# Performance work log

Measured on AMD Instinct MI355X. Metric: run time of the kernel, lower is better.

The kernel has to match this reference:

```python
import jax, jax.numpy as jnp
import numpy as np

N_NODES = 10000
N_EDGES = 80000
IN_DIM, HID, OUT_DIM, HEADS = 768, 512, 768, 4
NEG_SLOPE = 0.2


def setup_inputs() -> dict:
    key = jax.random.key(0)
    ks = jax.random.split(key, 10)
    g = 0.05
    return {
        "x": jax.random.normal(ks[0], (N_NODES, IN_DIM), jnp.float32),
        "edge_index": jax.random.randint(ks[1], (2, N_EDGES), 0, N_NODES, jnp.int64),
        # layer 1: GATConv(768 -> 512, heads=4, concat=True)
        "W1": jax.random.normal(ks[2], (IN_DIM, HEADS * HID), jnp.float32) * g,
        "a1_src": jax.random.normal(ks[3], (HEADS, HID), jnp.float32) * g,
        "a1_dst": jax.random.normal(ks[4], (HEADS, HID), jnp.float32) * g,
        "b1": jnp.zeros((HEADS * HID,), jnp.float32),
        # layer 2: GATConv(2048 -> 768, heads=1, concat=False)
        "W2": jax.random.normal(ks[5], (HEADS * HID, OUT_DIM), jnp.float32) * g,
        "a2_src": jax.random.normal(ks[6], (1, OUT_DIM), jnp.float32) * g,
        "a2_dst": jax.random.normal(ks[7], (1, OUT_DIM), jnp.float32) * g,
        "b2": jnp.zeros((OUT_DIM,), jnp.float32),
    }


def _gat_layer(x, src, dst, W, a_src, a_dst, b, heads, d_out, concat):
    N = x.shape[0]
    h = (x @ W).reshape(N, heads, d_out)              # [N, H, D]
    as_n = jnp.einsum('nhd,hd->nh', h, a_src)          # [N, H]
    ad_n = jnp.einsum('nhd,hd->nh', h, a_dst)
    e = jax.nn.leaky_relu(as_n[src] + ad_n[dst], NEG_SLOPE)  # [E, H]
    # segment softmax over destination nodes
    e_max = jax.lax.stop_gradient(jax.ops.segment_max(e, dst, num_segments=N))
    ex = jnp.exp(e - e_max[dst])
    denom = jax.ops.segment_sum(ex, dst, num_segments=N)
    alpha = ex / (denom[dst] + 1e-16)                  # [E, H]
    msg = alpha[:, :, None] * h[src]                   # [E, H, D]
    out = jax.ops.segment_sum(msg, dst, num_segments=N)  # [N, H, D]
    out = out.reshape(N, heads * d_out) if concat else out.mean(axis=1)
    return out + b


def reference(x, edge_index, W1, a1_src, a1_dst, b1, W2, a2_src, a2_dst, b2):
    N = x.shape[0]
    # PyG GATConv default: add self-loops
    loops = jnp.arange(N, dtype=edge_index.dtype)
    src = jnp.concatenate([edge_index[0], loops])
    dst = jnp.concatenate([edge_index[1], loops])
    h = _gat_layer(x, src, dst, W1, a1_src, a1_dst, b1, HEADS, HID, True)
    h = jax.nn.elu(h)
    out = _gat_layer(h, src, dst, W2, a2_src, a2_dst, b2, 1, OUT_DIM, False)
    return out
```

## Files before the change

kernel.cpp:

```cpp
#include <hip/hip_runtime.h>
#include <hip/hip_bf16.h>

#define N_NODES 10000
#define E_REAL  80000
#define E_TOTAL 90000
#define IN_DIM  768
#define HID     512
#define HEADS   4
#define OUT_DIM 768
#define HD1     (HEADS * HID)
#define NEG_SLOPE 0.2f
#define H1_HSTRIDE (N_NODES * HID)

typedef unsigned short ushort_t;
typedef unsigned int uint_t;

__device__ inline float b2f(ushort_t u) { return __uint_as_float(((uint_t)u) << 16); }
__device__ inline ushort_t f2b(float f) {
    __hip_bfloat16 h = __float2bfloat16(f);
    return *reinterpret_cast<ushort_t*>(&h);
}

__device__ inline void edge_sd(const int* __restrict__ ei, int e, int& s, int& d) {
    if (e < E_REAL) { s = ei[e]; d = ei[E_REAL + e]; }
    else            { s = e - E_REAL; d = s; }
}

#define GLDS(g, l) __builtin_amdgcn_global_load_lds( \
    (const __attribute__((address_space(1))) void*)(g), \
    (__attribute__((address_space(3))) void*)(l), 16, 0, 0)

static const long B_H1B  = 0L;
static const long B_HB   = 40960000L;
static const long B_XB   = 81920000L;
static const long B_W1T  = 97280000L;
static const long B_W2T  = 100425728L;
static const long B_SM   = 103571456L;
static const long SM_AS1   = 0;
static const long SM_AD1   = 40000;
static const long SM_DEN1  = 120000;
static const long SM_E1    = 160000;
static const long SM_AS2   = 520000;
static const long SM_AD2   = 530000;
static const long SM_DEN2  = 550000;
static const long SM_E2    = 560000;
static const long SM_CNT   = 650000;
static const long SM_ROWS  = 660000;
static const long SM_CURS  = 670016;
static const long SM_END   = 680032;
static const long B_CSRS = B_SM + SM_END * 4;
static const long B_CSRE = B_CSRS + 360000L;

__global__ __launch_bounds__(256)
void cast_bf16(const float* __restrict__ in, ushort_t* __restrict__ o, long n) {
    long i = ((long)blockIdx.x * 256 + threadIdx.x) * 8;
    if (i >= n) return;
    float4 v0 = *(const float4*)(in + i);
    float4 v1 = *(const float4*)(in + i + 4);
    ushort_t r[8] = {f2b(v0.x), f2b(v0.y), f2b(v0.z), f2b(v0.w),
                     f2b(v1.x), f2b(v1.y), f2b(v1.z), f2b(v1.w)};
    *(uint4*)(o + i) = *(uint4*)r;
}

__global__ __launch_bounds__(256)
void cast_transpose(const float* __restrict__ W, ushort_t* __restrict__ WT,
                    int K, int N) {
    __shared__ ushort_t t[32][33];
    const int n0 = blockIdx.x * 32, k0 = blockIdx.y * 32;
    const int tx = threadIdx.x & 31, ty = threadIdx.x >> 5;
#pragma unroll
    for (int i = 0; i < 4; ++i) {
        int k = ty + i * 8;
        t[k][tx] = f2b(W[(long)(k0 + k) * N + n0 + tx]);
    }
    __syncthreads();
#pragma unroll
    for (int i = 0; i < 4; ++i) {
        int n = ty + i * 8;
        WT[(long)(n0 + n) * K + k0 + tx] = t[tx][n];
    }
}

typedef short bf16x8 __attribute__((ext_vector_type(8)));
typedef float f32x4 __attribute__((ext_vector_type(4)));

#define BM 128
#define BN 128
#define BK 32

template<int CMODE>
__global__ __launch_bounds__(256)
void gemm_bf16(const ushort_t* __restrict__ A, const ushort_t* __restrict__ BT,
               ushort_t* __restrict__ C, int M, int N, int K) {
    __shared__ ushort_t As[BM * BK];
    __shared__ ushort_t Bs[BN * BK];
    const int tid  = threadIdx.x;
    const int wave = tid >> 6, lane = tid & 63;
    const int quad = lane >> 4, l16 = lane & 15;
    const int bm = blockIdx.y * BM, bn = blockIdx.x * BN;
    const int wr = (wave >> 1) * 64, wc = (wave & 1) * 64;

    const int ch0 = wave * 128 + lane;
    const int ch1 = ch0 + 64;
    const int r0 = ch0 >> 2, c0 = (ch0 & 3) ^ ((r0 >> 1) & 3);
    const int r1 = ch1 >> 2, c1 = (ch1 & 3) ^ ((r1 >> 1) & 3);
    const ushort_t* a0 = A + (long)(bm + r0) * K + c0 * 8;
    const ushort_t* a1 = A + (long)(bm + r1) * K + c1 * 8;
    const ushort_t* b0 = BT + (long)(bn + r0) * K + c0 * 8;
    const ushort_t* b1 = BT + (long)(bn + r1) * K + c1 * 8;
    ushort_t* lA0 = As + (wave * 128) * 8;
    ushort_t* lA1 = As + (wave * 128 + 64) * 8;
    ushort_t* lB0 = Bs + (wave * 128) * 8;
    ushort_t* lB1 = Bs + (wave * 128 + 64) * 8;

    const int swz = (l16 >> 1) & 3;
    f32x4 acc[4][4] = {};

    for (int k0 = 0; k0 < K; k0 += BK) {
        GLDS(a0 + k0, lA0);
        GLDS(a1 + k0, lA1);
        GLDS(b0 + k0, lB0);
        GLDS(b1 + k0, lB1);
        __syncthreads();
        bf16x8 af[4], bfr[4];
#pragma unroll
        for (int i = 0; i < 4; ++i) {
            af[i]  = *(const bf16x8*)(As + ((wr + i * 16 + l16) * 4 + (quad ^ swz)) * 8);
            bfr[i] = *(const bf16x8*)(Bs + ((wc + i * 16 + l16) * 4 + (quad ^ swz)) * 8);
        }
#pragma unroll
        for (int i = 0; i < 4; ++i)
#pragma unroll
            for (int j = 0; j < 4; ++j)
                acc[i][j] = __builtin_amdgcn_mfma_f32_16x16x32_bf16(
                    af[i], bfr[j], acc[i][j], 0, 0, 0);
        __syncthreads();
    }

#pragma unroll
    for (int i = 0; i < 4; ++i) {
#pragma unroll
        for (int r = 0; r < 4; ++r) {
            int row = bm + wr + i * 16 + quad * 4 + r;
            if (row >= M) continue;
#pragma unroll
            for (int j = 0; j < 4; ++j) {
                int col = bn + wc + j * 16 + l16;
                if (CMODE == 0) {
                    C[(long)row * N + col] = f2b(acc[i][j][r]);
                } else {
                    C[(long)(col >> 9) * H1_HSTRIDE + (long)row * HID + (col & 511)]
                        = f2b(acc[i][j][r]);
                }
            }
        }
    }
}

__global__ __launch_bounds__(256)
void attn1(const ushort_t* __restrict__ h, const float* __restrict__ a_s,
           const float* __restrict__ a_d, float* __restrict__ os,
           float* __restrict__ od) {
    const int n = blockIdx.x;
    const int w = threadIdx.x >> 6, lane = threadIdx.x & 63;
    uint4 hv = *(const uint4*)(h + (long)w * H1_HSTRIDE + (long)n * HID + lane * 8);
    const float* asp = a_s + w * HID + lane * 8;
    const float* adp = a_d + w * HID + lane * 8;
    const ushort_t* pb = (const ushort_t*)&hv;
    float ps = 0.f, pd = 0.f;
#pragma unroll
    for (int c = 0; c < 8; ++c) {
        float v = b2f(pb[c]);
        ps += v * asp[c];
        pd += v * adp[c];
    }
#pragma unroll
    for (int off = 32; off > 0; off >>= 1) {
        ps += __shfl_down(ps, off);
        pd += __shfl_down(pd, off);
    }
    if (lane == 0) { os[n * HEADS + w] = ps; od[n * HEADS + w] = pd; }
}

__global__ __launch_bounds__(256)
void attn2(const ushort_t* __restrict__ h, const float* __restrict__ a_s,
           const float* __restrict__ a_d, float* __restrict__ os,
           float* __restrict__ od) {
    __shared__ float rs[4], rd[4];
    const int n = blockIdx.x, tid = threadIdx.x;
    const int w = tid >> 6, lane = tid & 63;
    float ps = 0.f, pd = 0.f;
#pragma unroll
    for (int j = 0; j < 3; ++j) {
        int c = tid + j * 256;
        float v = b2f(h[(long)n * OUT_DIM + c]);
        ps += v * a_s[c];
        pd += v * a_d[c];
    }
#pragma unroll
    for (int off = 32; off > 0; off >>= 1) {
        ps += __shfl_down(ps, off);
        pd += __shfl_down(pd, off);
    }
    if (lane == 0) { rs[w] = ps; rd[w] = pd; }
    __syncthreads();
    if (tid == 0) {
        os[n] = rs[0] + rs[1] + rs[2] + rs[3];
        od[n] = rd[0] + rd[1] + rd[2] + rd[3];
    }
}

__global__ __launch_bounds__(256)
void edge_soft(const int* __restrict__ ei, int H,
               const float* __restrict__ as_n, const float* __restrict__ ad_n,
               float* __restrict__ ebuf, float* __restrict__ denom) {
    int idx = blockIdx.x * 256 + threadIdx.x;
    if (idx >= E_TOTAL * H) return;
    int e = idx / H, hh = idx - e * H;
    int s, d; edge_sd(ei, e, s, d);
    float v = as_n[(long)s * H + hh] + ad_n[(long)d * H + hh];
    v = v > 0.f ? v : NEG_SLOPE * v;
    float ex = expf(v);
    ebuf[idx] = ex;
    atomicAdd(&denom[(long)d * H + hh], ex);
}

__global__ __launch_bounds__(256)
void hist_dst(const int* __restrict__ ei, int* __restrict__ cnt) {
    int e = blockIdx.x * 256 + threadIdx.x;
    if (e >= E_TOTAL) return;
    int s, d; edge_sd(ei, e, s, d);
    atomicAdd(&cnt[d], 1);
}

#define SCAN_CH 40
__global__ __launch_bounds__(256)
void scan_nodes(const int* __restrict__ cnt, int* __restrict__ rows,
                int* __restrict__ curs) {
    __shared__ int part[256];
    const int tid = threadIdx.x;
    const int base = tid * SCAN_CH;
    int local[SCAN_CH];
    int sum = 0;
#pragma unroll
    for (int i = 0; i < SCAN_CH; ++i) {
        int idx = base + i;
        int v = (idx < N_NODES) ? cnt[idx] : 0;
        local[i] = v; sum += v;
    }
    part[tid] = sum;
    __syncthreads();
    for (int off = 1; off < 256; off <<= 1) {
        int v = (tid >= off) ? part[tid - off] : 0;
        __syncthreads();
        part[tid] += v;
        __syncthreads();
    }
    int run = part[tid] - sum;
#pragma unroll
    for (int i = 0; i < SCAN_CH; ++i) {
        int idx = base + i;
        if (idx < N_NODES) { rows[idx] = run; curs[idx] = run; run += local[i]; }
    }
    if (tid == 255) rows[N_NODES] = run;
}

__global__ __launch_bounds__(256)
void scatter_edges(const int* __restrict__ ei, int* __restrict__ curs,
                   int* __restrict__ csr_src, int* __restrict__ csr_eid) {
    int e = blockIdx.x * 256 + threadIdx.x;
    if (e >= E_TOTAL) return;
    int s, d; edge_sd(ei, e, s, d);
    int pos = atomicAdd(&curs[d], 1);
    csr_src[pos] = s;
    csr_eid[pos] = e;
}

__global__ __launch_bounds__(64)
void agg1(const int* __restrict__ rows, const int* __restrict__ csr_src,
          const int* __restrict__ csr_eid, const float* __restrict__ ebuf,
          const float* __restrict__ denom, const ushort_t* __restrict__ hf,
          const float* __restrict__ b1, ushort_t* __restrict__ o) {
    const int n = blockIdx.x, hh = blockIdx.y, lane = threadIdx.x;
    const int beg = rows[n], end = rows[n + 1];
    const ushort_t* hsl = hf + (long)hh * H1_HSTRIDE;
    const float dinv = 1.f / (denom[(long)n * HEADS + hh] + 1e-16f);
    float acc[8] = {};
    for (int k = beg; k < end; k += 4) {
        int nk = end - k; if (nk > 4) nk = 4;
        uint4 v[4]; float al[4];
#pragma unroll
        for (int u = 0; u < 4; ++u) {
            if (u < nk) {
                int s = csr_src[k + u];
                al[u] = ebuf[(long)csr_eid[k + u] * HEADS + hh] * dinv;
                v[u]  = *(const uint4*)(hsl + (long)s * HID + lane * 8);
            }
        }
#pragma unroll
        for (int u = 0; u < 4; ++u) {
            if (u < nk) {
                const ushort_t* p = (const ushort_t*)&v[u];
#pragma unroll
                for (int c = 0; c < 8; ++c) acc[c] += al[u] * b2f(p[c]);
            }
        }
    }
    const float* bp = b1 + hh * HID + lane * 8;
    ushort_t r[8];
#pragma unroll
    for (int c = 0; c < 8; ++c) {
        float vv = acc[c] + bp[c];
        r[c] = f2b(vv > 0.f ? vv : expm1f(vv));
    }
    *(uint4*)(o + (long)n * HD1 + hh * HID + lane * 8) = *(uint4*)r;
}

__global__ __launch_bounds__(64)
void agg2(const int* __restrict__ rows, const int* __restrict__ csr_src,
          const int* __restrict__ csr_eid, const float* __restrict__ ebuf,
          const float* __restrict__ denom, const ushort_t* __restrict__ hf,
          const float* __restrict__ b2, float* __restrict__ out) {
    const int n = blockIdx.x, lane = threadIdx.x;
    const int beg = rows[n], end = rows[n + 1];
    const float dinv = 1.f / (denom[n] + 1e-16f);
    float acc[12] = {};
    for (int k = beg; k < end; k += 4) {
        int nk = end - k; if (nk > 4) nk = 4;
        uint4 v4[4]; uint2 v2[4]; float al[4];
#pragma unroll
        for (int u = 0; u < 4; ++u) {
            if (u < nk) {
                int s = csr_src[k + u];
                al[u] = ebuf[csr_eid[k + u]] * dinv;
                const ushort_t* hp = hf + (long)s * OUT_DIM;
                v4[u] = *(const uint4*)(hp + lane * 8);
                v2[u] = *(const uint2*)(hp + 512 + lane * 4);
            }
        }
#pragma unroll
        for (int u = 0; u < 4; ++u) {
            if (u < nk) {
                const ushort_t* p4 = (const ushort_t*)&v4[u];
                const ushort_t* p2 = (const ushort_t*)&v2[u];
#pragma unroll
                for (int c = 0; c < 8; ++c) acc[c] += al[u] * b2f(p4[c]);
#pragma unroll
                for (int c = 0; c < 4; ++c) acc[8 + c] += al[u] * b2f(p2[c]);
            }
        }
    }
    float* op = out + (long)n * OUT_DIM;
#pragma unroll
    for (int c = 0; c < 8; ++c) op[lane * 8 + c] = acc[c] + b2[lane * 8 + c];
#pragma unroll
    for (int c = 0; c < 4; ++c)
        op[512 + lane * 4 + c] = acc[8 + c] + b2[512 + lane * 4 + c];
}

extern "C" void kernel_launch(void* const* d_in, const int* in_sizes, int n_in,
                              void* d_out, int out_size, void* d_ws, size_t ws_size,
                              hipStream_t stream) {
    const float* x   = (const float*)d_in[0];
    const int*   ei  = (const int*)d_in[1];
    const float* W1  = (const float*)d_in[2];
    const float* a1s = (const float*)d_in[3];
    const float* a1d = (const float*)d_in[4];
    const float* b1  = (const float*)d_in[5];
    const float* W2  = (const float*)d_in[6];
    const float* a2s = (const float*)d_in[7];
    const float* a2d = (const float*)d_in[8];
    const float* b2  = (const float*)d_in[9];
    float* out = (float*)d_out;
    char* base = (char*)d_ws;

    ushort_t* h1b = (ushort_t*)(base + B_H1B);
    ushort_t* hb  = (ushort_t*)(base + B_HB);
    ushort_t* xb  = (ushort_t*)(base + B_XB);
    ushort_t* h2b = xb;
    ushort_t* w1t = (ushort_t*)(base + B_W1T);
    ushort_t* w2t = (ushort_t*)(base + B_W2T);
    float*    sm  = (float*)(base + B_SM);

    float* as1  = sm + SM_AS1;
    float* ad1  = sm + SM_AD1;
    float* den1 = sm + SM_DEN1;
    float* e1   = sm + SM_E1;
    float* as2  = sm + SM_AS2;
    float* ad2  = sm + SM_AD2;
    float* den2 = sm + SM_DEN2;
    float* e2   = sm + SM_E2;
    int* cnt    = (int*)(sm + SM_CNT);
    int* rows   = (int*)(sm + SM_ROWS);
    int* curs   = (int*)(sm + SM_CURS);
    int* csr_src = (int*)(base + B_CSRS);
    int* csr_eid = (int*)(base + B_CSRE);

    hipMemsetAsync(sm, 0, (size_t)(SM_CNT + 10000) * sizeof(float), stream);

    {
        long nx = (long)N_NODES * IN_DIM;
        cast_bf16<<<(int)(nx / 8 / 256 + 1), 256, 0, stream>>>(x, xb, nx);
        cast_transpose<<<dim3(HD1 / 32, IN_DIM / 32), 256, 0, stream>>>(W1, w1t, IN_DIM, HD1);
        cast_transpose<<<dim3(OUT_DIM / 32, HD1 / 32), 256, 0, stream>>>(W2, w2t, HD1, OUT_DIM);
        hist_dst<<<(E_TOTAL + 255) / 256, 256, 0, stream>>>(ei, cnt);
        scan_nodes<<<1, 256, 0, stream>>>(cnt, rows, curs);
        scatter_edges<<<(E_TOTAL + 255) / 256, 256, 0, stream>>>(ei, curs, csr_src, csr_eid);
    }

    gemm_bf16<1><<<dim3(HD1 / BN, (N_NODES + BM - 1) / BM), 256, 0, stream>>>(
        xb, w1t, h1b, N_NODES, HD1, IN_DIM);
    attn1<<<N_NODES, 256, 0, stream>>>(h1b, a1s, a1d, as1, ad1);
    {
        int total = E_TOTAL * HEADS;
        edge_soft<<<(total + 255) / 256, 256, 0, stream>>>(ei, HEADS, as1, ad1, e1, den1);
    }
    agg1<<<dim3(N_NODES, HEADS), 64, 0, stream>>>(rows, csr_src, csr_eid, e1, den1, h1b, b1, hb);

    gemm_bf16<0><<<dim3(OUT_DIM / BN, (N_NODES + BM - 1) / BM), 256, 0, stream>>>(
        hb, w2t, h2b, N_NODES, OUT_DIM, HD1);
    attn2<<<N_NODES, 256, 0, stream>>>(h2b, a2s, a2d, as2, ad2);
    {
        int total = E_TOTAL;
        edge_soft<<<(total + 255) / 256, 256, 0, stream>>>(ei, 1, as2, ad2, e2, den2);
    }
    agg2<<<N_NODES, 64, 0, stream>>>(rows, csr_src, csr_eid, e2, den2, h2b, b2, out);
}
```

Measured before the change: 364.8 us.

## Split GAT aggregation across edge groups and feature slices with shuffle reduction

Both aggregation kernels now place four nodes in each 256-thread block, one wave per node. Each wave splits into four 16-lane groups that take interleaved edges, and the blocks are also split across feature slices (4 slices for layer 1, 8 for layer 2). Partial sums are combined with cross-lane shuffles before one group writes the result. The aim is more memory-level parallelism per node and better occupancy for the gather-heavy loops, at the cost of more blocks re-reading CSR indices and attention weights, and of idle lanes in layer 2 (only 12 of 16 lanes active).

```diff
diff --git a/kernel.cpp b/kernel.cpp
--- a/kernel.cpp
+++ b/kernel.cpp
@@ -276,86 +276,80 @@
     csr_eid[pos] = e;
 }
 
-__global__ __launch_bounds__(64)
+__global__ __launch_bounds__(256)
 void agg1(const int* __restrict__ rows, const int* __restrict__ csr_src,
           const int* __restrict__ csr_eid, const float* __restrict__ ebuf,
           const float* __restrict__ denom, const ushort_t* __restrict__ hf,
           const float* __restrict__ b1, ushort_t* __restrict__ o) {
-    const int n = blockIdx.x, hh = blockIdx.y, lane = threadIdx.x;
+    const int sh = blockIdx.x & 3, nq = blockIdx.x >> 2;
+    const int hh = blockIdx.y;
+    const int wave = threadIdx.x >> 6, lane = threadIdx.x & 63;
+    const int grp = lane >> 4, l = lane & 15;
+    const int n = nq * 4 + wave;
     const int beg = rows[n], end = rows[n + 1];
-    const ushort_t* hsl = hf + (long)hh * H1_HSTRIDE;
+    const ushort_t* hsl = hf + (long)hh * H1_HSTRIDE + sh * 128;
     const float dinv = 1.f / (denom[(long)n * HEADS + hh] + 1e-16f);
     float acc[8] = {};
-    for (int k = beg; k < end; k += 4) {
-        int nk = end - k; if (nk > 4) nk = 4;
-        uint4 v[4]; float al[4];
-#pragma unroll
-        for (int u = 0; u < 4; ++u) {
-            if (u < nk) {
-                int s = csr_src[k + u];
-                al[u] = ebuf[(long)csr_eid[k + u] * HEADS + hh] * dinv;
-                v[u]  = *(const uint4*)(hsl + (long)s * HID + lane * 8);
-            }
+    for (int k = beg + grp; k < end; k += 4) {
+        int s = csr_src[k];
+        float al = ebuf[(long)csr_eid[k] * HEADS + hh] * dinv;
+        uint4 v = *(const uint4*)(hsl + (long)s * HID + l * 8);
+        const ushort_t* p = (const ushort_t*)&v;
+#pragma unroll
+        for (int c = 0; c < 8; ++c) acc[c] += al * b2f(p[c]);
+    }
+#pragma unroll
+    for (int c = 0; c < 8; ++c) {
+        acc[c] += __shfl_down(acc[c], 32);
+        acc[c] += __shfl_down(acc[c], 16);
+    }
+    if (grp == 0) {
+        const int ch = hh * HID + sh * 128 + l * 8;
+        const float* bp = b1 + ch;
+        ushort_t r[8];
+#pragma unroll
+        for (int c = 0; c < 8; ++c) {
+            float vv = acc[c] + bp[c];
+            r[c] = f2b(vv > 0.f ? vv : expm1f(vv));
         }
-#pragma unroll
-        for (int u = 0; u < 4; ++u) {
-            if (u < nk) {
-                const ushort_t* p = (const ushort_t*)&v[u];
-#pragma unroll
-                for (int c = 0; c < 8; ++c) acc[c] += al[u] * b2f(p[c]);
-            }
-        }
-    }
-    const float* bp = b1 + hh * HID + lane * 8;
-    ushort_t r[8];
-#pragma unroll
-    for (int c = 0; c < 8; ++c) {
-        float vv = acc[c] + bp[c];
-        r[c] = f2b(vv > 0.f ? vv : expm1f(vv));
-    }
-    *(uint4*)(o + (long)n * HD1 + hh * HID + lane * 8) = *(uint4*)r;
-}
-
-__global__ __launch_bounds__(64)
+        *(uint4*)(o + (long)n * HD1 + ch) = *(uint4*)r;
+    }
+}
+
+__global__ __launch_bounds__(256)
 void agg2(const int* __restrict__ rows, const int* __restrict__ csr_src,
           const int* __restrict__ csr_eid, const float* __restrict__ ebuf,
           const float* __restrict__ denom, const ushort_t* __restrict__ hf,
           const float* __restrict__ b2, float* __restrict__ out) {
-    const int n = blockIdx.x, lane = threadIdx.x;
+    const int sh = blockIdx.x & 7, nq = blockIdx.x >> 3;
+    const int wave = threadIdx.x >> 6, lane = threadIdx.x & 63;
+    const int grp = lane >> 4, l = lane & 15;
+    const int lc = l < 12 ? l : 0;
+    const int n = nq * 4 + wave;
     const int beg = rows[n], end = rows[n + 1];
+    const ushort_t* hsl = hf + sh * 96;
     const float dinv = 1.f / (denom[n] + 1e-16f);
-    float acc[12] = {};
-    for (int k = beg; k < end; k += 4) {
-        int nk = end - k; if (nk > 4) nk = 4;
-        uint4 v4[4]; uint2 v2[4]; float al[4];
-#pragma unroll
-        for (int u = 0; u < 4; ++u) {
-            if (u < nk) {
-                int s = csr_src[k + u];
-                al[u] = ebuf[csr_eid[k + u]] * dinv;
-                const ushort_t* hp = hf + (long)s * OUT_DIM;
-                v4[u] = *(const uint4*)(hp + lane * 8);
-                v2[u] = *(const uint2*)(hp + 512 + lane * 4);
-            }
-        }
-#pragma unroll
-        for (int u = 0; u < 4; ++u) {
-            if (u < nk) {
-                const ushort_t* p4 = (const ushort_t*)&v4[u];
-                const ushort_t* p2 = (const ushort_t*)&v2[u];
-#pragma unroll
-                for (int c = 0; c < 8; ++c) acc[c] += al[u] * b2f(p4[c]);
-#pragma unroll
-                for (int c = 0; c < 4; ++c) acc[8 + c] += al[u] * b2f(p2[c]);
-            }
-        }
-    }
-    float* op = out + (long)n * OUT_DIM;
-#pragma unroll
-    for (int c = 0; c < 8; ++c) op[lane * 8 + c] = acc[c] + b2[lane * 8 + c];
-#pragma unroll
-    for (int c = 0; c < 4; ++c)
-        op[512 + lane * 4 + c] = acc[8 + c] + b2[512 + lane * 4 + c];
+    float acc[8] = {};
+    for (int k = beg + grp; k < end; k += 4) {
+        int s = csr_src[k];
+        float al = ebuf[csr_eid[k]] * dinv;
+        uint4 v = *(const uint4*)(hsl + (long)s * OUT_DIM + lc * 8);
+        const ushort_t* p = (const ushort_t*)&v;
+#pragma unroll
+        for (int c = 0; c < 8; ++c) acc[c] += al * b2f(p[c]);
+    }
+#pragma unroll
+    for (int c = 0; c < 8; ++c) {
+        acc[c] += __shfl_down(acc[c], 32);
+        acc[c] += __shfl_down(acc[c], 16);
+    }
+    if (grp == 0 && l < 12) {
+        const int ch = sh * 96 + l * 8;
+        float* op = out + (long)n * OUT_DIM + ch;
+        const float* bp = b2 + ch;
+#pragma unroll
+        for (int c = 0; c < 8; ++c) op[c] = acc[c] + bp[c];
+    }
 }
 
 extern "C" void kernel_launch(void* const* d_in, const int* in_sizes, int n_in,
@@ -415,7 +409,8 @@
         int total = E_TOTAL * HEADS;
         edge_soft<<<(total + 255) / 256, 256, 0, stream>>>(ei, HEADS, as1, ad1, e1, den1);
     }
-    agg1<<<dim3(N_NODES, HEADS), 64, 0, stream>>>(rows, csr_src, csr_eid, e1, den1, h1b, b1, hb);
+    agg1<<<dim3((N_NODES / 4) * 4, HEADS), 256, 0, stream>>>(
+        rows, csr_src, csr_eid, e1, den1, h1b, b1, hb);
 
     gemm_bf16<0><<<dim3(OUT_DIM / BN, (N_NODES + BM - 1) / BM), 256, 0, stream>>>(
         hb, w2t, h2b, N_NODES, OUT_DIM, HD1);
@@ -424,5 +419,6 @@
         int total = E_TOTAL;
         edge_soft<<<(total + 255) / 256, 256, 0, stream>>>(ei, 1, as2, ad2, e2, den2);
     }
-    agg2<<<N_NODES, 64, 0, stream>>>(rows, csr_src, csr_eid, e2, den2, h2b, b2, out);
-}
+    agg2<<<(N_NODES / 4) * 8, 256, 0, stream>>>(
+        rows, csr_src, csr_eid, e2, den2, h2b, b2, out);
+}
```

New measurement: 453.9 us. 24.4% more time.

## Fuse edge softmax into CSR aggregation kernels, dropping edge_soft and atomics

Applied to the files above, without the earlier changes.

Removes the separate edge_soft kernels, which wrote per-edge exp scores and accumulated denominators with atomics. Each aggregation block now computes the leaky-relu exp score for its incoming edges on the fly, sums the denominator locally and normalises once at the end. This also drops the csr_eid array and shrinks the memset. The per-edge exp is recomputed redundantly by all 64 lanes, and it switches to the faster, less accurate __expf. Like before, there is no max subtraction.

```diff
diff --git a/kernel.cpp b/kernel.cpp
--- a/kernel.cpp
+++ b/kernel.cpp
@@ -38,18 +38,13 @@
 static const long B_SM   = 103571456L;
 static const long SM_AS1   = 0;
 static const long SM_AD1   = 40000;
-static const long SM_DEN1  = 120000;
-static const long SM_E1    = 160000;
-static const long SM_AS2   = 520000;
-static const long SM_AD2   = 530000;
-static const long SM_DEN2  = 550000;
-static const long SM_E2    = 560000;
-static const long SM_CNT   = 650000;
-static const long SM_ROWS  = 660000;
-static const long SM_CURS  = 670016;
-static const long SM_END   = 680032;
+static const long SM_AS2   = 80000;
+static const long SM_AD2   = 90000;
+static const long SM_CNT   = 100000;
+static const long SM_ROWS  = 110000;
+static const long SM_CURS  = 120016;
+static const long SM_END   = 130016;
 static const long B_CSRS = B_SM + SM_END * 4;
-static const long B_CSRE = B_CSRS + 360000L;
 
 __global__ __launch_bounds__(256)
 void cast_bf16(const float* __restrict__ in, ushort_t* __restrict__ o, long n) {
@@ -211,21 +206,6 @@
 }
 
 __global__ __launch_bounds__(256)
-void edge_soft(const int* __restrict__ ei, int H,
-               const float* __restrict__ as_n, const float* __restrict__ ad_n,
-               float* __restrict__ ebuf, float* __restrict__ denom) {
-    int idx = blockIdx.x * 256 + threadIdx.x;
-    if (idx >= E_TOTAL * H) return;
-    int e = idx / H, hh = idx - e * H;
-    int s, d; edge_sd(ei, e, s, d);
-    float v = as_n[(long)s * H + hh] + ad_n[(long)d * H + hh];
-    v = v > 0.f ? v : NEG_SLOPE * v;
-    float ex = expf(v);
-    ebuf[idx] = ex;
-    atomicAdd(&denom[(long)d * H + hh], ex);
-}
-
-__global__ __launch_bounds__(256)
 void hist_dst(const int* __restrict__ ei, int* __restrict__ cnt) {
     int e = blockIdx.x * 256 + threadIdx.x;
     if (e >= E_TOTAL) return;
@@ -267,50 +247,54 @@
 
 __global__ __launch_bounds__(256)
 void scatter_edges(const int* __restrict__ ei, int* __restrict__ curs,
-                   int* __restrict__ csr_src, int* __restrict__ csr_eid) {
+                   int* __restrict__ csr_src) {
     int e = blockIdx.x * 256 + threadIdx.x;
     if (e >= E_TOTAL) return;
     int s, d; edge_sd(ei, e, s, d);
     int pos = atomicAdd(&curs[d], 1);
     csr_src[pos] = s;
-    csr_eid[pos] = e;
 }
 
 __global__ __launch_bounds__(64)
 void agg1(const int* __restrict__ rows, const int* __restrict__ csr_src,
-          const int* __restrict__ csr_eid, const float* __restrict__ ebuf,
-          const float* __restrict__ denom, const ushort_t* __restrict__ hf,
-          const float* __restrict__ b1, ushort_t* __restrict__ o) {
+          const float* __restrict__ as_n, const float* __restrict__ ad_n,
+          const ushort_t* __restrict__ hf, const float* __restrict__ b1,
+          ushort_t* __restrict__ o) {
     const int n = blockIdx.x, hh = blockIdx.y, lane = threadIdx.x;
     const int beg = rows[n], end = rows[n + 1];
     const ushort_t* hsl = hf + (long)hh * H1_HSTRIDE;
-    const float dinv = 1.f / (denom[(long)n * HEADS + hh] + 1e-16f);
+    const float adv = ad_n[(long)n * HEADS + hh];
     float acc[8] = {};
+    float dsum = 0.f;
     for (int k = beg; k < end; k += 4) {
         int nk = end - k; if (nk > 4) nk = 4;
-        uint4 v[4]; float al[4];
+        uint4 v[4]; float ex[4];
 #pragma unroll
         for (int u = 0; u < 4; ++u) {
             if (u < nk) {
                 int s = csr_src[k + u];
-                al[u] = ebuf[(long)csr_eid[k + u] * HEADS + hh] * dinv;
+                float sc = as_n[(long)s * HEADS + hh] + adv;
+                sc = sc > 0.f ? sc : NEG_SLOPE * sc;
+                ex[u] = __expf(sc);
                 v[u]  = *(const uint4*)(hsl + (long)s * HID + lane * 8);
             }
         }
 #pragma unroll
         for (int u = 0; u < 4; ++u) {
             if (u < nk) {
+                dsum += ex[u];
                 const ushort_t* p = (const ushort_t*)&v[u];
 #pragma unroll
-                for (int c = 0; c < 8; ++c) acc[c] += al[u] * b2f(p[c]);
+                for (int c = 0; c < 8; ++c) acc[c] += ex[u] * b2f(p[c]);
             }
         }
     }
+    const float dinv = 1.f / (dsum + 1e-16f);
     const float* bp = b1 + hh * HID + lane * 8;
     ushort_t r[8];
 #pragma unroll
     for (int c = 0; c < 8; ++c) {
-        float vv = acc[c] + bp[c];
+        float vv = acc[c] * dinv + bp[c];
         r[c] = f2b(vv > 0.f ? vv : expm1f(vv));
     }
     *(uint4*)(o + (long)n * HD1 + hh * HID + lane * 8) = *(uint4*)r;
@@ -318,21 +302,24 @@
 
 __global__ __launch_bounds__(64)
 void agg2(const int* __restrict__ rows, const int* __restrict__ csr_src,
-          const int* __restrict__ csr_eid, const float* __restrict__ ebuf,
-          const float* __restrict__ denom, const ushort_t* __restrict__ hf,
-          const float* __restrict__ b2, float* __restrict__ out) {
+          const float* __restrict__ as_n, const float* __restrict__ ad_n,
+          const ushort_t* __restrict__ hf, const float* __restrict__ b2,
+          float* __restrict__ out) {
     const int n = blockIdx.x, lane = threadIdx.x;
     const int beg = rows[n], end = rows[n + 1];
-    const float dinv = 1.f / (denom[n] + 1e-16f);
+    const float adv = ad_n[n];
     float acc[12] = {};
+    float dsum = 0.f;
     for (int k = beg; k < end; k += 4) {
         int nk = end - k; if (nk > 4) nk = 4;
-        uint4 v4[4]; uint2 v2[4]; float al[4];
+        uint4 v4[4]; uint2 v2[4]; float ex[4];
 #pragma unroll
         for (int u = 0; u < 4; ++u) {
             if (u < nk) {
                 int s = csr_src[k + u];
-                al[u] = ebuf[csr_eid[k + u]] * dinv;
+                float sc = as_n[s] + adv;
+                sc = sc > 0.f ? sc : NEG_SLOPE * sc;
+                ex[u] = __expf(sc);
                 const ushort_t* hp = hf + (long)s * OUT_DIM;
                 v4[u] = *(const uint4*)(hp + lane * 8);
                 v2[u] = *(const uint2*)(hp + 512 + lane * 4);
@@ -341,21 +328,24 @@
 #pragma unroll
         for (int u = 0; u < 4; ++u) {
             if (u < nk) {
+                dsum += ex[u];
                 const ushort_t* p4 = (const ushort_t*)&v4[u];
                 const ushort_t* p2 = (const ushort_t*)&v2[u];
 #pragma unroll
-                for (int c = 0; c < 8; ++c) acc[c] += al[u] * b2f(p4[c]);
-#pragma unroll
-                for (int c = 0; c < 4; ++c) acc[8 + c] += al[u] * b2f(p2[c]);
+                for (int c = 0; c < 8; ++c) acc[c] += ex[u] * b2f(p4[c]);
+#pragma unroll
+                for (int c = 0; c < 4; ++c) acc[8 + c] += ex[u] * b2f(p2[c]);
             }
         }
     }
+    const float dinv = 1.f / (dsum + 1e-16f);
     float* op = out + (long)n * OUT_DIM;
 #pragma unroll
-    for (int c = 0; c < 8; ++c) op[lane * 8 + c] = acc[c] + b2[lane * 8 + c];
+    for (int c = 0; c < 8; ++c)
+        op[lane * 8 + c] = acc[c] * dinv + b2[lane * 8 + c];
 #pragma unroll
     for (int c = 0; c < 4; ++c)
-        op[512 + lane * 4 + c] = acc[8 + c] + b2[512 + lane * 4 + c];
+        op[512 + lane * 4 + c] = acc[8 + c] * dinv + b2[512 + lane * 4 + c];
 }
 
 extern "C" void kernel_launch(void* const* d_in, const int* in_sizes, int n_in,
@@ -384,19 +374,14 @@
 
     float* as1  = sm + SM_AS1;
     float* ad1  = sm + SM_AD1;
-    float* den1 = sm + SM_DEN1;
-    float* e1   = sm + SM_E1;
     float* as2  = sm + SM_AS2;
     float* ad2  = sm + SM_AD2;
-    float* den2 = sm + SM_DEN2;
-    float* e2   = sm + SM_E2;
     int* cnt    = (int*)(sm + SM_CNT);
     int* rows   = (int*)(sm + SM_ROWS);
     int* curs   = (int*)(sm + SM_CURS);
     int* csr_src = (int*)(base + B_CSRS);
-    int* csr_eid = (int*)(base + B_CSRE);
-
-    hipMemsetAsync(sm, 0, (size_t)(SM_CNT + 10000) * sizeof(float), stream);
+
+    hipMemsetAsync(cnt, 0, 10000 * sizeof(int), stream);
 
     {
         long nx = (long)N_NODES * IN_DIM;
@@ -405,24 +390,18 @@
         cast_transpose<<<dim3(OUT_DIM / 32, HD1 / 32), 256, 0, stream>>>(W2, w2t, HD1, OUT_DIM);
         hist_dst<<<(E_TOTAL + 255) / 256, 256, 0, stream>>>(ei, cnt);
         scan_nodes<<<1, 256, 0, stream>>>(cnt, rows, curs);
-        scatter_edges<<<(E_TOTAL + 255) / 256, 256, 0, stream>>>(ei, curs, csr_src, csr_eid);
+        scatter_edges<<<(E_TOTAL + 255) / 256, 256, 0, stream>>>(ei, curs, csr_src);
     }
 
     gemm_bf16<1><<<dim3(HD1 / BN, (N_NODES + BM - 1) / BM), 256, 0, stream>>>(
         xb, w1t, h1b, N_NODES, HD1, IN_DIM);
     attn1<<<N_NODES, 256, 0, stream>>>(h1b, a1s, a1d, as1, ad1);
-    {
-        int total = E_TOTAL * HEADS;
-        edge_soft<<<(total + 255) / 256, 256, 0, stream>>>(ei, HEADS, as1, ad1, e1, den1);
-    }
-    agg1<<<dim3(N_NODES, HEADS), 64, 0, stream>>>(rows, csr_src, csr_eid, e1, den1, h1b, b1, hb);
+    agg1<<<dim3(N_NODES, HEADS), 64, 0, stream>>>(
+        rows, csr_src, as1, ad1, h1b, b1, hb);
 
     gemm_bf16<0><<<dim3(OUT_DIM / BN, (N_NODES + BM - 1) / BM), 256, 0, stream>>>(
         hb, w2t, h2b, N_NODES, OUT_DIM, HD1);
     attn2<<<N_NODES, 256, 0, stream>>>(h2b, a2s, a2d, as2, ad2);
-    {
-        int total = E_TOTAL;
-        edge_soft<<<(total + 255) / 256, 256, 0, stream>>>(ei, 1, as2, ad2, e2, den2);
-    }
-    agg2<<<N_NODES, 64, 0, stream>>>(rows, csr_src, csr_eid, e2, den2, h2b, b2, out);
-}
+    agg2<<<N_NODES, 64, 0, stream>>>(
+        rows, csr_src, as2, ad2, h2b, b2, out);
+}
```

New measurement: 343.8 us. 5.8% less time.
